# Kernel tuning notes

Hardware: AMD Instinct MI355X
Metric: run time of the kernel (lower is better)

The kernel has to match this reference:

```python
import jax, jax.numpy as jnp
from jax import lax
import numpy as np

IN, H, T, NCLS = 256, 16, 10, 2
BN_EPS = 1e-5
NEG_SLOPE = 0.01


def _lstm_layer(x, w_ih, w_hh, b_ih, b_hh):
    # x: [B, T, D]; w_ih: [4H, D]; w_hh: [4H, H]; gates in torch order i,f,g,o
    B = x.shape[0]
    xg = jnp.einsum('btd,gd->btg', x, w_ih) + b_ih + b_hh  # [B, T, 4H]
    def step(carry, xt):
        h, c = carry
        g = xt + h @ w_hh.T
        i, f, gg, o = jnp.split(g, 4, axis=-1)
        c = jax.nn.sigmoid(f) * c + jax.nn.sigmoid(i) * jnp.tanh(gg)
        h = jax.nn.sigmoid(o) * jnp.tanh(c)
        return (h, c), h
    h0 = jnp.zeros((B, H), x.dtype)
    _, hs = lax.scan(step, (h0, h0), jnp.swapaxes(xg, 0, 1))  # [T, B, H]
    return jnp.swapaxes(hs, 0, 1)  # [B, T, H]


def setup_inputs() -> dict:
    key = jax.random.key(0)
    ks = jax.random.split(key, 12)
    s_ih0 = 1.0 / np.sqrt(IN); s_h = 1.0 / np.sqrt(H)
    inp = {
        'inputs': jax.random.normal(ks[0], (16384, T, IN), jnp.float32),
        'agegender': jax.random.normal(ks[1], (16384, 2), jnp.float32),
        # layer 0
        'w_ih0': jax.random.uniform(ks[2], (4 * H, IN), jnp.float32, -s_h, s_h),
        'w_hh0': jax.random.uniform(ks[3], (4 * H, H), jnp.float32, -s_h, s_h),
        'b_ih0': jax.random.uniform(ks[4], (4 * H,), jnp.float32, -s_h, s_h),
        'b_hh0': jax.random.uniform(ks[5], (4 * H,), jnp.float32, -s_h, s_h),
        # layer 1
        'w_ih1': jax.random.uniform(ks[6], (4 * H, H), jnp.float32, -s_h, s_h),
        'w_hh1': jax.random.uniform(ks[7], (4 * H, H), jnp.float32, -s_h, s_h),
        'b_ih1': jax.random.uniform(ks[8], (4 * H,), jnp.float32, -s_h, s_h),
        'b_hh1': jax.random.uniform(ks[9], (4 * H,), jnp.float32, -s_h, s_h),
        # BN(160) and FC(162 -> 2)
        'bn_gamma': jnp.ones((T * H,), jnp.float32),
        'bn_beta': jnp.zeros((T * H,), jnp.float32),
        'fc_w': jax.random.uniform(ks[10], (NCLS, T * H + 2), jnp.float32, -1.0 / np.sqrt(T * H + 2), 1.0 / np.sqrt(T * H + 2)),
        'fc_b': jax.random.uniform(ks[11], (NCLS,), jnp.float32, -1.0 / np.sqrt(T * H + 2), 1.0 / np.sqrt(T * H + 2)),
    }
    return inp


def reference(inputs, agegender, w_ih0, w_hh0, b_ih0, b_hh0,
              w_ih1, w_hh1, b_ih1, b_hh1, bn_gamma, bn_beta, fc_w, fc_b):
    h1 = _lstm_layer(inputs, w_ih0, w_hh0, b_ih0, b_hh0)   # [B, T, H]
    h2 = _lstm_layer(h1, w_ih1, w_hh1, b_ih1, b_hh1)       # [B, T, H]
    flat = h2.reshape(h2.shape[0], -1)                      # [B, 160]
    # BatchNorm1d in training mode: biased batch statistics
    mean = jnp.mean(flat, axis=0)
    var = jnp.var(flat, axis=0)
    xn = (flat - mean) * lax.rsqrt(var + BN_EPS) * bn_gamma + bn_beta
    act = jnp.where(xn >= 0, xn, NEG_SLOPE * xn)            # LeakyReLU
    cat = jnp.concatenate([act, agegender], axis=1)         # [B, 162]
    logits = cat @ fc_w.T + fc_b
    return jax.nn.softmax(logits, axis=1)
```

## Files before the change

kernel.cpp:

```cpp
#include <hip/hip_runtime.h>

#define NB 16384
#define TT 10
#define DIN 256
#define HH 16
#define NG 64
#define NF 160

typedef __attribute__((ext_vector_type(8))) _Float16 half8;
typedef __attribute__((ext_vector_type(4))) _Float16 half4;
typedef __attribute__((ext_vector_type(4))) float f32x4;

__device__ __forceinline__ float sigf(float x) { return 1.0f / (1.0f + __expf(-x)); }
__device__ __forceinline__ float tanhf_(float x) {
    float e = __expf(2.0f * x);
    return 1.0f - 2.0f / (e + 1.0f);
}

__global__ __launch_bounds__(256, 1) void k_mega(
        const float* __restrict__ x, const float* __restrict__ wih0,
        const float* __restrict__ bih0, const float* __restrict__ bhh0,
        const float* __restrict__ whh0, const float* __restrict__ wih1,
        const float* __restrict__ whh1, const float* __restrict__ bi1,
        const float* __restrict__ bh1, _Float16* __restrict__ flatT) {
    __shared__ half8 Bl[2048];
    const int tid = threadIdx.x;
    const int l = tid & 63;
    const int wv = tid >> 6;

    #pragma unroll
    for (int q = 0; q < 8; ++q) {
        const int fi = q * 256 + tid;
        const int c = fi >> 9;
        const int s = (fi >> 6) & 7;
        const int ll = fi & 63;
        const int row = c * 16 + (ll & 15);
        const int k0 = s * 32 + ((ll >> 4) << 3);
        const float* wp = wih0 + (size_t)row * DIN + k0;
        float4 a = *(const float4*)wp;
        float4 b = *(const float4*)(wp + 4);
        half8 h;
        h[0] = (_Float16)a.x; h[1] = (_Float16)a.y;
        h[2] = (_Float16)a.z; h[3] = (_Float16)a.w;
        h[4] = (_Float16)b.x; h[5] = (_Float16)b.y;
        h[6] = (_Float16)b.z; h[7] = (_Float16)b.w;
        Bl[fi] = h;
    }

    half4 w0f[4], w1f[4], w2f[4];
    f32x4 b0[4], b1[4];
    #pragma unroll
    for (int c = 0; c < 4; ++c) {
        const int mrow = c * 16 + (l & 15);
        const int mk = (l >> 4) << 2;
        float4 v0 = *(const float4*)(whh0 + (size_t)mrow * HH + mk);
        w0f[c][0] = (_Float16)v0.x; w0f[c][1] = (_Float16)v0.y;
        w0f[c][2] = (_Float16)v0.z; w0f[c][3] = (_Float16)v0.w;
        float4 v1 = *(const float4*)(wih1 + (size_t)mrow * HH + mk);
        w1f[c][0] = (_Float16)v1.x; w1f[c][1] = (_Float16)v1.y;
        w1f[c][2] = (_Float16)v1.z; w1f[c][3] = (_Float16)v1.w;
        float4 v2 = *(const float4*)(whh1 + (size_t)mrow * HH + mk);
        w2f[c][0] = (_Float16)v2.x; w2f[c][1] = (_Float16)v2.y;
        w2f[c][2] = (_Float16)v2.z; w2f[c][3] = (_Float16)v2.w;
        const int bofs = c * 16 + mk;
        float4 vi0 = *(const float4*)(bih0 + bofs);
        float4 vh0 = *(const float4*)(bhh0 + bofs);
        b0[c][0] = vi0.x + vh0.x; b0[c][1] = vi0.y + vh0.y;
        b0[c][2] = vi0.z + vh0.z; b0[c][3] = vi0.w + vh0.w;
        float4 vi1 = *(const float4*)(bi1 + bofs);
        float4 vh1 = *(const float4*)(bh1 + bofs);
        b1[c][0] = vi1.x + vh1.x; b1[c][1] = vi1.y + vh1.y;
        b1[c][2] = vi1.z + vh1.z; b1[c][3] = vi1.w + vh1.w;
    }
    __syncthreads();

    const int sb = blockIdx.x * 4 + wv;
    const float* xp = x + (size_t)(sb * 16 + (l & 15)) * TT * DIN + ((l >> 4) << 3);

    f32x4 A0[8], B0[8], A1[8], B1[8];
    #pragma unroll
    for (int s = 0; s < 8; ++s) {
        A0[s] = *(const f32x4*)(xp + s * 32);
        B0[s] = *(const f32x4*)(xp + s * 32 + 4);
    }

    half4 h0f, h1f;
    #pragma unroll
    for (int j = 0; j < 4; ++j) { h0f[j] = (_Float16)0.0f; h1f[j] = (_Float16)0.0f; }
    f32x4 cs0 = (f32x4)0.0f, cs1 = (f32x4)0.0f;

#define STEP(t, CA, CB, NA, NB2)                                               \
    {                                                                          \
        if ((t) < 9) {                                                         \
            _Pragma("unroll")                                                  \
            for (int s = 0; s < 8; ++s) {                                      \
                NA[s] = *(const f32x4*)(xp + ((t) + 1) * DIN + s * 32);        \
                NB2[s] = *(const f32x4*)(xp + ((t) + 1) * DIN + s * 32 + 4);   \
            }                                                                  \
        }                                                                      \
        f32x4 ac0[4] = {b0[0], b0[1], b0[2], b0[3]};                           \
        _Pragma("unroll")                                                      \
        for (int s = 0; s < 8; ++s) {                                          \
            float fv[8] = {CA[s].x, CA[s].y, CA[s].z, CA[s].w,                 \
                           CB[s].x, CB[s].y, CB[s].z, CB[s].w};                \
            half8 xh, xl;                                                      \
            _Pragma("unroll")                                                  \
            for (int j = 0; j < 8; ++j) {                                      \
                _Float16 hi = (_Float16)fv[j];                                 \
                xh[j] = hi;                                                    \
                xl[j] = (_Float16)(fv[j] - (float)hi);                         \
            }                                                                  \
            _Pragma("unroll")                                                  \
            for (int c = 0; c < 4; ++c) {                                      \
                half8 wf = Bl[(c * 8 + s) * 64 + l];                           \
                ac0[c] = __builtin_amdgcn_mfma_f32_16x16x32_f16(wf, xh, ac0[c], 0, 0, 0); \
                ac0[c] = __builtin_amdgcn_mfma_f32_16x16x32_f16(wf, xl, ac0[c], 0, 0, 0); \
            }                                                                  \
        }                                                                      \
        _Pragma("unroll")                                                      \
        for (int c = 0; c < 4; ++c)                                            \
            ac0[c] = __builtin_amdgcn_mfma_f32_16x16x16f16(w0f[c], h0f, ac0[c], 0, 0, 0); \
        f32x4 h0v;                                                             \
        _Pragma("unroll")                                                      \
        for (int r = 0; r < 4; ++r) {                                          \
            float iv = sigf(ac0[0][r]), fg = sigf(ac0[1][r]);                  \
            float gv = tanhf_(ac0[2][r]), ov = sigf(ac0[3][r]);                \
            cs0[r] = fg * cs0[r] + iv * gv;                                    \
            h0v[r] = ov * tanhf_(cs0[r]);                                      \
        }                                                                      \
        h0f[0] = (_Float16)h0v[0]; h0f[1] = (_Float16)h0v[1];                  \
        h0f[2] = (_Float16)h0v[2]; h0f[3] = (_Float16)h0v[3];                  \
        f32x4 ac1[4] = {b1[0], b1[1], b1[2], b1[3]};                           \
        _Pragma("unroll")                                                      \
        for (int c = 0; c < 4; ++c) {                                          \
            ac1[c] = __builtin_amdgcn_mfma_f32_16x16x16f16(w1f[c], h0f, ac1[c], 0, 0, 0); \
            ac1[c] = __builtin_amdgcn_mfma_f32_16x16x16f16(w2f[c], h1f, ac1[c], 0, 0, 0); \
        }                                                                      \
        f32x4 h1v;                                                             \
        _Pragma("unroll")                                                      \
        for (int r = 0; r < 4; ++r) {                                          \
            float iv = sigf(ac1[0][r]), fg = sigf(ac1[1][r]);                  \
            float gv = tanhf_(ac1[2][r]), ov = sigf(ac1[3][r]);                \
            cs1[r] = fg * cs1[r] + iv * gv;                                    \
            h1v[r] = ov * tanhf_(cs1[r]);                                      \
        }                                                                      \
        h1f[0] = (_Float16)h1v[0]; h1f[1] = (_Float16)h1v[1];                  \
        h1f[2] = (_Float16)h1v[2]; h1f[3] = (_Float16)h1v[3];                  \
        _Pragma("unroll")                                                      \
        for (int r = 0; r < 4; ++r)                                            \
            flatT[(size_t)((t) * 16 + ((l >> 4) << 2) + r) * NB + sb * 16 + (l & 15)] = (_Float16)h1v[r]; \
    }

    STEP(0, A0, B0, A1, B1)
    STEP(1, A1, B1, A0, B0)
    STEP(2, A0, B0, A1, B1)
    STEP(3, A1, B1, A0, B0)
    STEP(4, A0, B0, A1, B1)
    STEP(5, A1, B1, A0, B0)
    STEP(6, A0, B0, A1, B1)
    STEP(7, A1, B1, A0, B0)
    STEP(8, A0, B0, A1, B1)
    STEP(9, A1, B1, A0, B0)
#undef STEP
}

__global__ __launch_bounds__(256) void k_bn(
        const _Float16* __restrict__ flatT, const float* __restrict__ gamma,
        const float* __restrict__ beta, float* __restrict__ scale,
        float* __restrict__ shift) {
    const int f = blockIdx.x;
    const int tid = threadIdx.x;
    const _Float16* col = flatT + (size_t)f * NB;
    float s = 0.0f, q = 0.0f;
    #pragma unroll 8
    for (int i = tid; i < NB; i += 256) {
        float v = (float)col[i];
        s += v; q += v * v;
    }
    #pragma unroll
    for (int o = 32; o > 0; o >>= 1) {
        s += __shfl_down(s, o, 64);
        q += __shfl_down(q, o, 64);
    }
    __shared__ float rs[4], rq[4];
    const int wv = tid >> 6;
    if ((tid & 63) == 0) { rs[wv] = s; rq[wv] = q; }
    __syncthreads();
    if (tid == 0) {
        float S = rs[0] + rs[1] + rs[2] + rs[3];
        float Q = rq[0] + rq[1] + rq[2] + rq[3];
        float mean = S * (1.0f / NB);
        float var = Q * (1.0f / NB) - mean * mean;
        float sc = gamma[f] * rsqrtf(var + 1e-5f);
        scale[f] = sc;
        shift[f] = beta[f] - mean * sc;
    }
}

__global__ __launch_bounds__(256) void k_fc(
        const _Float16* __restrict__ flatT, const float* __restrict__ scale,
        const float* __restrict__ shift, const float* __restrict__ ag,
        const float* __restrict__ fcw, const float* __restrict__ fcb,
        float* __restrict__ out) {
    const int smp = blockIdx.x * 256 + threadIdx.x;
    float p0 = 0.0f, p1 = 0.0f;
    #pragma unroll 8
    for (int f = 0; f < NF; ++f) {
        float xn = (float)flatT[(size_t)f * NB + smp] * scale[f] + shift[f];
        float a = xn >= 0.0f ? xn : 0.01f * xn;
        p0 += a * fcw[f];
        p1 += a * fcw[162 + f];
    }
    float a0 = ag[(size_t)smp * 2 + 0], a1 = ag[(size_t)smp * 2 + 1];
    float l0 = p0 + a0 * fcw[160] + a1 * fcw[161] + fcb[0];
    float l1 = p1 + a0 * fcw[162 + 160] + a1 * fcw[162 + 161] + fcb[1];
    float m = fmaxf(l0, l1);
    float e0 = __expf(l0 - m), e1 = __expf(l1 - m);
    float inv = 1.0f / (e0 + e1);
    out[(size_t)smp * 2 + 0] = e0 * inv;
    out[(size_t)smp * 2 + 1] = e1 * inv;
}

extern "C" void kernel_launch(void* const* d_in, const int* in_sizes, int n_in,
                              void* d_out, int out_size, void* d_ws, size_t ws_size,
                              hipStream_t stream) {
    const float* x     = (const float*)d_in[0];
    const float* ag    = (const float*)d_in[1];
    const float* wih0  = (const float*)d_in[2];
    const float* whh0  = (const float*)d_in[3];
    const float* bih0  = (const float*)d_in[4];
    const float* bhh0  = (const float*)d_in[5];
    const float* wih1  = (const float*)d_in[6];
    const float* whh1  = (const float*)d_in[7];
    const float* bih1  = (const float*)d_in[8];
    const float* bhh1  = (const float*)d_in[9];
    const float* gamma = (const float*)d_in[10];
    const float* beta  = (const float*)d_in[11];
    const float* fcw   = (const float*)d_in[12];
    const float* fcb   = (const float*)d_in[13];
    float* out = (float*)d_out;

    float* ws = (float*)d_ws;
    _Float16* flatT = (_Float16*)ws;
    float* scale = ws + 1310720;
    float* shift = ws + 1310880;

    k_mega<<<dim3(256), dim3(256), 0, stream>>>(x, wih0, bih0, bhh0, whh0,
                                                wih1, whh1, bih1, bhh1, flatT);
    k_bn<<<dim3(NF),    dim3(256), 0, stream>>>(flatT, gamma, beta, scale, shift);
    k_fc<<<dim3(64),    dim3(256), 0, stream>>>(flatT, scale, shift, ag, fcw, fcb, out);
}
```

Measured before the change: 54.25 us.

## Stage LSTM input timesteps through LDS with async global_load_lds double buffering

```diff
diff --git a/kernel.cpp b/kernel.cpp
--- a/kernel.cpp
+++ b/kernel.cpp
@@ -10,7 +10,13 @@
 typedef __attribute__((ext_vector_type(8))) _Float16 half8;
 typedef __attribute__((ext_vector_type(4))) _Float16 half4;
 typedef __attribute__((ext_vector_type(4))) float f32x4;
-
+typedef unsigned int u32;
+
+__device__ __forceinline__ void gld16(const float* g, float* l) {
+    __builtin_amdgcn_global_load_lds(
+        (const __attribute__((address_space(1))) u32*)g,
+        (__attribute__((address_space(3))) u32*)l, 16, 0, 0);
+}
 __device__ __forceinline__ float sigf(float x) { return 1.0f / (1.0f + __expf(-x)); }
 __device__ __forceinline__ float tanhf_(float x) {
     float e = __expf(2.0f * x);
@@ -24,6 +30,7 @@
         const float* __restrict__ whh1, const float* __restrict__ bi1,
         const float* __restrict__ bh1, _Float16* __restrict__ flatT) {
     __shared__ half8 Bl[2048];
+    __shared__ float xs[4][2][2048];
     const int tid = threadIdx.x;
     const int l = tid & 63;
     const int wv = tid >> 6;
@@ -75,34 +82,43 @@
     __syncthreads();
 
     const int sb = blockIdx.x * 4 + wv;
-    const float* xp = x + (size_t)(sb * 16 + (l & 15)) * TT * DIN + ((l >> 4) << 3);
-
-    f32x4 A0[8], B0[8], A1[8], B1[8];
-    #pragma unroll
-    for (int s = 0; s < 8; ++s) {
-        A0[s] = *(const f32x4*)(xp + s * 32);
-        B0[s] = *(const f32x4*)(xp + s * 32 + 4);
-    }
+    float* xsbuf = &xs[wv][0][0];
+    const int lsmp = l & 15;
+    const int rswz = (lsmp & 7) << 4;
 
     half4 h0f, h1f;
     #pragma unroll
     for (int j = 0; j < 4; ++j) { h0f[j] = (_Float16)0.0f; h1f[j] = (_Float16)0.0f; }
     f32x4 cs0 = (f32x4)0.0f, cs1 = (f32x4)0.0f;
 
-#define STEP(t, CA, CB, NA, NB2)                                               \
+#define ISSUE(t, c)                                                            \
     {                                                                          \
-        if ((t) < 9) {                                                         \
-            _Pragma("unroll")                                                  \
-            for (int s = 0; s < 8; ++s) {                                      \
-                NA[s] = *(const f32x4*)(xp + ((t) + 1) * DIN + s * 32);        \
-                NB2[s] = *(const f32x4*)(xp + ((t) + 1) * DIN + s * 32 + 4);   \
-            }                                                                  \
-        }                                                                      \
-        f32x4 ac0[4] = {b0[0], b0[1], b0[2], b0[3]};                           \
-        _Pragma("unroll")                                                      \
-        for (int s = 0; s < 8; ++s) {                                          \
-            float fv[8] = {CA[s].x, CA[s].y, CA[s].z, CA[s].w,                 \
-                           CB[s].x, CB[s].y, CB[s].z, CB[s].w};                \
+        float* dst = xsbuf + (c) * 2048;                                       \
+        _Pragma("unroll")                                                      \
+        for (int i = 0; i < 8; ++i) {                                          \
+            const int smp = 2 * i + (l >> 5);                                  \
+            const int inseg = ((l & 31) * 16) ^ ((smp & 7) << 4);              \
+            gld16(x + (size_t)(sb * 16 + smp) * (TT * DIN)                     \
+                    + (t) * DIN + (c) * 128 + (inseg >> 2),                    \
+                  dst + i * 256);                                              \
+        }                                                                      \
+    }
+
+#define WAITVM(n)                                                              \
+    asm volatile("s_waitcnt vmcnt(" #n ")" ::: "memory");                      \
+    __builtin_amdgcn_sched_barrier(0);
+#define FENCELGKM                                                              \
+    asm volatile("s_waitcnt lgkmcnt(0)" ::: "memory");                         \
+    __builtin_amdgcn_sched_barrier(0);
+
+#define CHUNK(c, s0base, ac0)                                                  \
+        _Pragma("unroll")                                                      \
+        for (int sp = 0; sp < 4; ++sp) {                                       \
+            const int woff = sp * 128 + ((l >> 4) << 5);                       \
+            const char* segp = (const char*)(xsbuf + (c) * 2048) + lsmp * 512; \
+            f32x4 va = *(const f32x4*)(segp + (woff ^ rswz));                  \
+            f32x4 vb = *(const f32x4*)(segp + ((woff + 16) ^ rswz));           \
+            float fv[8] = {va.x, va.y, va.z, va.w, vb.x, vb.y, vb.z, vb.w};    \
             half8 xh, xl;                                                      \
             _Pragma("unroll")                                                  \
             for (int j = 0; j < 8; ++j) {                                      \
@@ -111,12 +127,14 @@
                 xl[j] = (_Float16)(fv[j] - (float)hi);                         \
             }                                                                  \
             _Pragma("unroll")                                                  \
-            for (int c = 0; c < 4; ++c) {                                      \
-                half8 wf = Bl[(c * 8 + s) * 64 + l];                           \
-                ac0[c] = __builtin_amdgcn_mfma_f32_16x16x32_f16(wf, xh, ac0[c], 0, 0, 0); \
-                ac0[c] = __builtin_amdgcn_mfma_f32_16x16x32_f16(wf, xl, ac0[c], 0, 0, 0); \
+            for (int cc = 0; cc < 4; ++cc) {                                   \
+                half8 wf = Bl[(cc * 8 + (s0base) + sp) * 64 + l];              \
+                ac0[cc] = __builtin_amdgcn_mfma_f32_16x16x32_f16(wf, xh, ac0[cc], 0, 0, 0); \
+                ac0[cc] = __builtin_amdgcn_mfma_f32_16x16x32_f16(wf, xl, ac0[cc], 0, 0, 0); \
             }                                                                  \
-        }                                                                      \
+        }
+
+#define REC(t, ac0)                                                            \
         _Pragma("unroll")                                                      \
         for (int c = 0; c < 4; ++c)                                            \
             ac0[c] = __builtin_amdgcn_mfma_f32_16x16x16f16(w0f[c], h0f, ac0[c], 0, 0, 0); \
@@ -148,20 +166,41 @@
         h1f[2] = (_Float16)h1v[2]; h1f[3] = (_Float16)h1v[3];                  \
         _Pragma("unroll")                                                      \
         for (int r = 0; r < 4; ++r)                                            \
-            flatT[(size_t)((t) * 16 + ((l >> 4) << 2) + r) * NB + sb * 16 + (l & 15)] = (_Float16)h1v[r]; \
-    }
-
-    STEP(0, A0, B0, A1, B1)
-    STEP(1, A1, B1, A0, B0)
-    STEP(2, A0, B0, A1, B1)
-    STEP(3, A1, B1, A0, B0)
-    STEP(4, A0, B0, A1, B1)
-    STEP(5, A1, B1, A0, B0)
-    STEP(6, A0, B0, A1, B1)
-    STEP(7, A1, B1, A0, B0)
-    STEP(8, A0, B0, A1, B1)
-    STEP(9, A1, B1, A0, B0)
+            flatT[(size_t)((t) * 16 + ((l >> 4) << 2) + r) * NB + sb * 16 + lsmp] = (_Float16)h1v[r];
+
+#define STEP(t, WA, WB)                                                        \
+    {                                                                          \
+        f32x4 ac0[4] = {b0[0], b0[1], b0[2], b0[3]};                           \
+        WAITVM(WA)                                                             \
+        CHUNK(0, 0, ac0)                                                       \
+        FENCELGKM                                                              \
+        if ((t) < 9) ISSUE((t) + 1, 0)                                         \
+        WAITVM(WB)                                                             \
+        CHUNK(1, 4, ac0)                                                       \
+        FENCELGKM                                                              \
+        if ((t) < 9) ISSUE((t) + 1, 1)                                         \
+        REC(t, ac0)                                                            \
+    }
+
+    ISSUE(0, 0)
+    ISSUE(0, 1)
+
+    STEP(0, 8, 8)
+    STEP(1, 8, 8)
+    STEP(2, 8, 8)
+    STEP(3, 8, 8)
+    STEP(4, 8, 8)
+    STEP(5, 8, 8)
+    STEP(6, 8, 8)
+    STEP(7, 8, 8)
+    STEP(8, 8, 8)
+    STEP(9, 8, 0)
 #undef STEP
+#undef REC
+#undef CHUNK
+#undef ISSUE
+#undef WAITVM
+#undef FENCELGKM
 }
 
 __global__ __launch_bounds__(256) void k_bn(
```

After: 59.71 us. +10.1%, slower.
